# Optimization experiments

Measured on AMD Instinct MI355X. Metric: run time of the kernel, lower is better.

## Reference

```python
import jax, jax.numpy as jnp
import numpy as np
import math

B, LQ, S, D = 8, 4096, 77, 1024
H, HD = 16, 64
R, ALPHA = 192, 16.0
LORA_SCALE = ALPHA / R
N_SUBJ = 32


def setup_inputs() -> dict:
    key = jax.random.key(0)
    ks = jax.random.split(key, 16)
    w = 0.02
    return {
        "hidden_states": jax.random.normal(ks[0], (B, LQ, D), jnp.float32),
        "encoder_hidden_states": jax.random.normal(ks[1], (B, S, D), jnp.float32),
        "Wq": jax.random.normal(ks[2], (D, D), jnp.float32) * w,
        "Wk": jax.random.normal(ks[3], (D, D), jnp.float32) * w,
        "Wv": jax.random.normal(ks[4], (D, D), jnp.float32) * w,
        "Wo": jax.random.normal(ks[5], (D, D), jnp.float32) * w,
        "bo": jnp.zeros((D,), jnp.float32),
        "Ak": jax.random.normal(ks[6], (R, D), jnp.float32) * w,
        "Bk": jax.random.normal(ks[7], (D, R), jnp.float32) * w,
        "Av": jax.random.normal(ks[8], (R, D), jnp.float32) * w,
        "Bv": jax.random.normal(ks[9], (D, R), jnp.float32) * w,
        "Ao": jax.random.normal(ks[10], (R, D), jnp.float32) * w,
        "Bo": jax.random.normal(ks[11], (D, R), jnp.float32) * w,
        "cross_attn_scale_factor": jnp.ones((), jnp.float32),
        "subj_b": jax.random.randint(ks[12], (N_SUBJ,), 0, B, jnp.int32),
        "subj_n": jax.random.randint(ks[13], (N_SUBJ,), 0, S, jnp.int32),
    }


def _lora(x, A, Bm):
    # peft LoRA delta: scale * (x @ A^T) @ B^T
    return LORA_SCALE * ((x @ A.T) @ Bm.T)


def reference(hidden_states, encoder_hidden_states, Wq, Wk, Wv, Wo, bo,
              Ak, Bk, Av, Bv, Ao, Bo, cross_attn_scale_factor, subj_b, subj_n):
    hs, ehs = hidden_states, encoder_hidden_states
    # q_lora_updates_query=False -> query uses the base projection only
    q = hs @ Wq.T                                  # [B, LQ, D]
    k = ehs @ Wk.T + _lora(ehs, Ak, Bk)            # [B, S, D] (to_k_lora)
    v = ehs @ Wv.T + _lora(ehs, Av, Bv)            # [B, S, D] (to_v_lora)

    q = q.reshape(B, LQ, H, HD).transpose(0, 2, 1, 3)   # [B,H,LQ,HD]
    k = k.reshape(B, S, H, HD).transpose(0, 2, 1, 3)    # [B,H,S,HD]
    v = v.reshape(B, S, H, HD).transpose(0, 2, 1, 3)

    scale = 1.0 / math.sqrt(HD)
    attn_score = jnp.einsum('bhld,bhsd->bhls', q, k) * scale  # [B,H,LQ,S]

    # normalize_cross_attn: zero-center subject-token scores over query dim,
    # then rescale by the learned cross_attn_scale_factor.
    sub = attn_score[subj_b, :, :, subj_n]                    # [K,H,LQ]
    sub = (sub - sub.mean(axis=2, keepdims=True)) * cross_attn_scale_factor
    attn_score = attn_score.at[subj_b, :, :, subj_n].set(sub)

    attn_weight = jax.nn.softmax(attn_score, axis=-1)
    out = jnp.einsum('bhls,bhsd->bhld', attn_weight, v)       # [B,H,LQ,HD]
    out = out.transpose(0, 2, 1, 3).reshape(B, LQ, D)

    # to_out_lora: base out-proj (with bias) + LoRA delta; to_out[1] dropout = id
    out = out @ Wo.T + bo + _lora(out, Ao, Bo)
    return out
```

## Files before the change

kernel.cpp:

```cpp
#include <hip/hip_runtime.h>
#include <stdint.h>

#define B_     8
#define LQ_    4096
#define S_     77
#define SP_    80
#define D_     1024
#define H_     16
#define HD_    64
#define NC_    1280
#define NSUBJ_ 32

typedef __attribute__((ext_vector_type(4))) float  f4;
typedef __attribute__((ext_vector_type(8))) short  short8;
typedef __attribute__((ext_vector_type(8))) unsigned short us8;
typedef __attribute__((ext_vector_type(4))) unsigned short us4;

__device__ __forceinline__ unsigned short f2bf(float f) {
  union { float f; unsigned u; } x; x.f = f;
  unsigned r = x.u + 0x7FFFu + ((x.u >> 16) & 1u);
  return (unsigned short)(r >> 16);
}

__device__ __forceinline__ void gload16(const void* g, void* s) {
  __builtin_amdgcn_global_load_lds((const __attribute__((address_space(1))) void*)g,
                                   (__attribute__((address_space(3))) void*)s, 16, 0, 0);
}

__global__ __launch_bounds__(256) void k_hssum(const float* __restrict__ hs,
                                               float* __restrict__ part,
                                               unsigned short* __restrict__ hsb) {
  int b = blockIdx.y;
  size_t base = ((size_t)b * LQ_ + (size_t)blockIdx.x * 64) * D_ + threadIdx.x * 4;
  f4 acc = {0.f, 0.f, 0.f, 0.f};
  for (int l = 0; l < 64; ++l) {
    f4 v = *(const f4*)(hs + base + (size_t)l * D_);
    acc += v;
    if (hsb) {
      us4 o;
#pragma unroll
      for (int j = 0; j < 4; ++j) o[j] = f2bf(v[j]);
      *(us4*)(hsb + base + (size_t)l * D_) = o;
    }
  }
  *(f4*)(part + (size_t)blockIdx.x * (B_ * D_) + b * D_ + threadIdx.x * 4) = acc;
}

__global__ __launch_bounds__(256) void k_hsred(const float* __restrict__ part,
                                               float* __restrict__ hssum) {
  int i = blockIdx.x * 256 + threadIdx.x;
  float s = 0.f;
  for (int x = 0; x < 64; ++x) s += part[(size_t)x * (B_ * D_) + i];
  hssum[i] = s;
}

__global__ __launch_bounds__(256) void k_tr4(const float* __restrict__ Wq, const float* __restrict__ Ak,
                                             const float* __restrict__ Av, const float* __restrict__ Ao,
                                             float* __restrict__ wqT, float* __restrict__ akT,
                                             float* __restrict__ avT, float* __restrict__ aoT) {
  int z = blockIdx.z;
  const float* in = z == 0 ? Wq : (z == 1 ? Ak : (z == 2 ? Av : Ao));
  float* out = z == 0 ? wqT : (z == 1 ? akT : (z == 2 ? avT : aoT));
  int R = z == 0 ? 1024 : 192;
  const int C = 1024;
  int c0 = blockIdx.x * 32, r0 = blockIdx.y * 32;
  if (r0 >= R) return;
  __shared__ float tile[32][33];
  int tx = threadIdx.x & 31, ty = threadIdx.x >> 5;
#pragma unroll
  for (int k = 0; k < 4; ++k)
    tile[ty + 8 * k][tx] = in[(size_t)(r0 + ty + 8 * k) * C + c0 + tx];
  __syncthreads();
#pragma unroll
  for (int k = 0; k < 4; ++k)
    out[(size_t)(c0 + ty + 8 * k) * R + r0 + tx] = tile[tx][ty + 8 * k];
}

template <bool OBF>
__device__ __forceinline__ void gemm64_body(
    const float* __restrict__ A, int lda, const float* __restrict__ Bt, int ldb,
    void* __restrict__ Cv, int ldc, long cbase, const float* __restrict__ Dm, int ldd,
    int M, int Mv, int N, int K, float alpha, int m0, int n0,
    short* As, short* Bs) {
  int t = threadIdx.x, lane = t & 63, wid = t >> 6;
  int wm = wid >> 1, wn = wid & 1;
  f4 acc[2][2] = {};
  int srow = t >> 2, skc = (t & 3) * 8;
  for (int k0 = 0; k0 < K; k0 += 32) {
    __syncthreads();
    f4 a0 = {0,0,0,0}, a1 = {0,0,0,0}, b0 = {0,0,0,0}, b1 = {0,0,0,0};
    if (m0 + srow < Mv) {
      const float* p = A + (size_t)(m0 + srow) * lda + k0 + skc;
      a0 = *(const f4*)p; a1 = *(const f4*)(p + 4);
    }
    if (n0 + srow < N) {
      const float* p = Bt + (size_t)(n0 + srow) * ldb + k0 + skc;
      b0 = *(const f4*)p; b1 = *(const f4*)(p + 4);
    }
    us8 ua, ub;
#pragma unroll
    for (int j = 0; j < 4; ++j) {
      ua[j] = f2bf(a0[j]); ua[4 + j] = f2bf(a1[j]);
      ub[j] = f2bf(b0[j]); ub[4 + j] = f2bf(b1[j]);
    }
    *(us8*)(As + srow * 40 + skc) = ua;
    *(us8*)(Bs + srow * 40 + skc) = ub;
    __syncthreads();
    short8 fa[2], fb[2];
#pragma unroll
    for (int i = 0; i < 2; ++i) {
      fa[i] = *(const short8*)(As + (wm * 32 + i * 16 + (lane & 15)) * 40 + (lane >> 4) * 8);
      fb[i] = *(const short8*)(Bs + (wn * 32 + i * 16 + (lane & 15)) * 40 + (lane >> 4) * 8);
    }
#pragma unroll
    for (int mi = 0; mi < 2; ++mi)
#pragma unroll
      for (int ni = 0; ni < 2; ++ni)
        acc[mi][ni] = __builtin_amdgcn_mfma_f32_16x16x32_bf16(fa[mi], fb[ni], acc[mi][ni], 0, 0, 0);
  }
#pragma unroll
  for (int mi = 0; mi < 2; ++mi)
#pragma unroll
    for (int ni = 0; ni < 2; ++ni)
#pragma unroll
      for (int j = 0; j < 4; ++j) {
        int row = m0 + wm * 32 + mi * 16 + (lane >> 4) * 4 + j;
        int col = n0 + wn * 32 + ni * 16 + (lane & 15);
        if (row < M && col < N) {
          float val = acc[mi][ni][j] * alpha;
          if (Dm) val += Dm[(size_t)row * ldd + col];
          size_t idx = (size_t)cbase + (size_t)row * ldc + col;
          if (OBF) ((unsigned short*)Cv)[idx] = f2bf(val);
          else     ((float*)Cv)[idx] = val;
        }
      }
}

template <bool OBF>
__global__ __launch_bounds__(256) void k_gemm_small(
    const float* __restrict__ A, int lda, long sA1, long sA2,
    const float* __restrict__ Bt, int ldb, long sB1, long sB2,
    void* __restrict__ Cv, int ldc, long sC1, long sC2,
    const float* __restrict__ Dm, int ldd,
    int M, int Mv, int N, int K, float alpha, int Z2) {
  int z = blockIdx.z, z1 = z / Z2, z2 = z - z1 * Z2;
  __shared__ short As[64 * 40];
  __shared__ short Bs[64 * 40];
  gemm64_body<OBF>(A + z1 * sA1 + z2 * sA2, lda, Bt + z1 * sB1 + z2 * sB2, ldb,
                   Cv, ldc, z1 * sC1 + z2 * sC2, Dm, ldd, M, Mv, N, K, alpha,
                   blockIdx.x * 64, blockIdx.y * 64, As, Bs);
}

__global__ __launch_bounds__(256) void k_weff(
    const float* __restrict__ Bk, const float* __restrict__ Bv, const float* __restrict__ Bo,
    const float* __restrict__ akT, const float* __restrict__ avT, const float* __restrict__ aoT,
    const float* __restrict__ Wk, const float* __restrict__ Wv, const float* __restrict__ Wo,
    float* __restrict__ weff, float alpha) {
  int z = blockIdx.z;
  const float* A  = z == 0 ? Bk : (z == 1 ? Bv : Bo);
  const float* Bt = z == 0 ? akT : (z == 1 ? avT : aoT);
  const float* Dm = z == 0 ? Wk : (z == 1 ? Wv : Wo);
  __shared__ short As[64 * 40];
  __shared__ short Bs[64 * 40];
  gemm64_body<false>(A, 192, Bt, 192, weff + (size_t)z * 1048576, 1024, 0, Dm, 1024,
                     1024, 1024, 1024, 192, alpha, blockIdx.x * 64, blockIdx.y * 64, As, Bs);
}

__global__ void k_mubeta(const float* __restrict__ hssum, const float* __restrict__ Wq,
                         const float* __restrict__ kv,
                         const int* __restrict__ sb, const int* __restrict__ sn,
                         const float* __restrict__ csf_p,
                         float* __restrict__ alphav, float* __restrict__ betav) {
  int h = blockIdx.x, b = blockIdx.y;
  int t = threadIdx.x;
  __shared__ float qp[64];
  {
    int hd = t >> 1, half = t & 1;
    const float* wr = Wq + (size_t)(h * 64 + hd) * D_ + half * 512;
    const float* hp = hssum + b * D_ + half * 512;
    float s = 0.f;
    for (int d = 0; d < 512; d += 4) {
      f4 w = *(const f4*)(wr + d);
      f4 x = *(const f4*)(hp + d);
      s += w[0] * x[0] + w[1] * x[1] + w[2] * x[2] + w[3] * x[3];
    }
    s += __shfl_xor(s, 1, 64);
    if (half == 0) qp[hd] = s * (1.f / 4096.f);
  }
  __syncthreads();
  int s = t;
  if (s >= SP_) return;
  const float* kp = kv + ((size_t)(b * SP_ + s)) * 2048 + h * HD_;
  float mu = 0.f;
#pragma unroll 8
  for (int hd = 0; hd < HD_; ++hd) mu += qp[hd] * kp[hd];
  mu *= 0.125f;
  bool subj = false;
  for (int i = 0; i < NSUBJ_; ++i) subj = subj || (sb[i] == b && sn[i] == s);
  float csf = *csf_p;
  int c = b * NC_ + h * SP_ + s;
  alphav[c] = subj ? csf : 1.f;
  betav[c] = (s >= S_) ? -1e30f : (subj ? -mu * csf : 0.f);
}

__global__ __launch_bounds__(512, 2) void k_score_big(
    const unsigned short* __restrict__ hsb, const unsigned short* __restrict__ Mt,
    const float* __restrict__ alphav, const float* __restrict__ betav,
    unsigned short* __restrict__ P) {
  extern __shared__ short lds[];
  int id = blockIdx.x;
  int x = id & 7, idp = id >> 3;
  int nt = idp & 3;
  int pid = (idp >> 2) * 8 + x;
  int b = pid >> 4, mt = pid & 15;
  int m0 = mt * 256, n0 = nt * 320;

  const unsigned short* Ab = hsb + (size_t)b * LQ_ * D_;
  const unsigned short* Bb = Mt + (size_t)b * NC_ * D_;
  const float* alp = alphav + b * NC_;
  const float* bet = betav + b * NC_;
  unsigned short* Pb = P + (size_t)b * LQ_ * NC_;

  int t = threadIdx.x, lane = t & 63, wid = t >> 6;
  int wm = wid >> 2, wn = wid & 3;
  int r = lane & 15, q = lane >> 4;
  f4 acc[8][5] = {};

  auto SA = [&](int bf, int k0, int p) {
    int cb = p * 512 + wid * 64;
    int cc = cb + lane;
    int row = cc >> 2, gc = (cc & 3) ^ ((row >> 1) & 3);
    gload16(Ab + (size_t)(m0 + row) * D_ + k0 + gc * 8, (char*)(lds + bf * 8192) + cb * 16);
  };
  auto SB = [&](int bf, int k0, int p) {
    int cb = p * 512 + wid * 64;
    int cc = cb + lane;
    int row = cc >> 2, gc = (cc & 3) ^ ((row >> 1) & 3);
    gload16(Bb + (size_t)(n0 + row) * D_ + k0 + gc * 8, (char*)(lds + 32768 + bf * 10240) + cb * 16);
  };
  auto STAGE = [&](int bf, int k0) {
    SA(bf, k0, 0); SA(bf, k0, 1);
    SB(bf, k0, 0); SB(bf, k0, 1);
    if (wid < 4) { int cb = 1024 + wid * 64; int cc = cb + lane;
      int row = cc >> 2, gc = (cc & 3) ^ ((row >> 1) & 3);
      gload16(Bb + (size_t)(n0 + row) * D_ + k0 + gc * 8, (char*)(lds + 32768) + (size_t)bf * 20480 + cb * 16);
    }
  };

  const int T = 32;
  STAGE(0, 0); STAGE(1, 32); STAGE(2, 64);
  for (int kt = 0; kt < T; ++kt) {
    if (kt + 3 < T) {
      STAGE((kt + 3) & 3, (kt + 3) * 32);
      if (wid < 4) asm volatile("s_waitcnt vmcnt(15)" ::: "memory");
      else         asm volatile("s_waitcnt vmcnt(12)" ::: "memory");
    } else if (kt + 2 < T) {
      if (wid < 4) asm volatile("s_waitcnt vmcnt(10)" ::: "memory");
      else         asm volatile("s_waitcnt vmcnt(8)" ::: "memory");
    } else if (kt + 1 < T) {
      if (wid < 4) asm volatile("s_waitcnt vmcnt(5)" ::: "memory");
      else         asm volatile("s_waitcnt vmcnt(4)" ::: "memory");
    } else {
      asm volatile("s_waitcnt vmcnt(0)" ::: "memory");
    }
    __builtin_amdgcn_s_barrier();
    int cur = kt & 3;
    const short* Ar = lds + cur * 8192;
    const short* Br = lds + 32768 + cur * 10240;
    short8 fa[8], fb[5];
#pragma unroll
    for (int ni = 0; ni < 5; ++ni) {
      int row = wn * 80 + ni * 16 + r;
      fb[ni] = *(const short8*)(Br + row * 32 + ((q ^ ((row >> 1) & 3)) * 8));
    }
#pragma unroll
    for (int mi = 0; mi < 8; ++mi) {
      int row = wm * 128 + mi * 16 + r;
      fa[mi] = *(const short8*)(Ar + row * 32 + ((q ^ ((row >> 1) & 3)) * 8));
    }
    __builtin_amdgcn_s_setprio(1);
#pragma unroll
    for (int mi = 0; mi < 8; ++mi)
#pragma unroll
      for (int ni = 0; ni < 5; ++ni)
        acc[mi][ni] = __builtin_amdgcn_mfma_f32_16x16x32_bf16(fa[mi], fb[ni], acc[mi][ni], 0, 0, 0);
    __builtin_amdgcn_s_setprio(0);
    __builtin_amdgcn_s_barrier();
  }

  float al[5], be[5];
#pragma unroll
  for (int ni = 0; ni < 5; ++ni) {
    int cc = n0 + wn * 80 + ni * 16 + r;
    al[ni] = alp[cc]; be[ni] = bet[cc];
  }
#pragma unroll
  for (int mi = 0; mi < 8; ++mi) {
#pragma unroll
    for (int j = 0; j < 4; ++j) {
      float v[5];
      float m = -3.0e38f;
#pragma unroll
      for (int ni = 0; ni < 5; ++ni) { v[ni] = acc[mi][ni][j] * al[ni] + be[ni]; m = fmaxf(m, v[ni]); }
#pragma unroll
      for (int off = 1; off < 16; off <<= 1) m = fmaxf(m, __shfl_xor(m, off, 64));
      float ssum = 0.f;
#pragma unroll
      for (int ni = 0; ni < 5; ++ni) { v[ni] = __expf(v[ni] - m); ssum += v[ni]; }
#pragma unroll
      for (int off = 1; off < 16; off <<= 1) ssum += __shfl_xor(ssum, off, 64);
      float inv = 1.f / ssum;
      int row = m0 + wm * 128 + mi * 16 + q * 4 + j;
      size_t rb = (size_t)row * NC_ + n0 + wn * 80 + r;
#pragma unroll
      for (int ni = 0; ni < 5; ++ni)
        Pb[rb + ni * 16] = f2bf(v[ni] * inv);
    }
  }
}

__global__ __launch_bounds__(256) void k_score_f32(
    const float* __restrict__ hs, const unsigned short* __restrict__ Mt,
    const float* __restrict__ alphav, const float* __restrict__ betav,
    unsigned short* __restrict__ P) {
  int id = blockIdx.x;
  int x = id & 7, idp = id >> 3;
  int n_t = idp & 7;
  int pid = (idp >> 3) * 8 + x;
  int b = pid >> 5, m_t = pid & 31;
  int m0 = m_t * 128, n0 = n_t * 160;
  const float* Af = hs + (size_t)b * LQ_ * D_;
  const unsigned short* Bb = Mt + (size_t)b * NC_ * D_;
  const float* alp = alphav + b * NC_;
  const float* bet = betav + b * NC_;
  unsigned short* Pb = P + (size_t)b * LQ_ * NC_;
  __shared__ short As[128 * 64];
  __shared__ short Bs[160 * 64];
  int t = threadIdx.x, lane = t & 63, wid = t >> 6;
  int wm = wid >> 1, wn = wid & 1;
  int srow = lane >> 3;
  int schunk = (lane & 7) ^ srow;
  f4 acc[4][5] = {};
  for (int k0 = 0; k0 < D_; k0 += 64) {
    __syncthreads();
    for (int i = wid; i < 20; i += 4)
      gload16(Bb + (size_t)(n0 + i * 8 + srow) * D_ + k0 + schunk * 8, (char*)Bs + i * 1024);
    int arow = t >> 3, ac = t & 7;
    int awc = ac ^ (arow & 7);
#pragma unroll
    for (int p = 0; p < 4; ++p) {
      int row = p * 32 + arow;
      const float* src = Af + (size_t)(m0 + row) * D_ + k0 + ac * 8;
      f4 v0 = *(const f4*)src;
      f4 v1 = *(const f4*)(src + 4);
      us8 u;
#pragma unroll
      for (int j = 0; j < 4; ++j) { u[j] = f2bf(v0[j]); u[4 + j] = f2bf(v1[j]); }
      *(us8*)(As + row * 64 + awc * 8) = u;
    }
    __syncthreads();
#pragma unroll
    for (int kk = 0; kk < 2; ++kk) {
      int co = ((kk * 4 + (lane >> 4)) ^ (lane & 7)) * 8;
      short8 fa[4], fb[5];
#pragma unroll
      for (int mi = 0; mi < 4; ++mi)
        fa[mi] = *(const short8*)(As + (wm * 64 + mi * 16 + (lane & 15)) * 64 + co);
#pragma unroll
      for (int ni = 0; ni < 5; ++ni)
        fb[ni] = *(const short8*)(Bs + (wn * 80 + ni * 16 + (lane & 15)) * 64 + co);
#pragma unroll
      for (int mi = 0; mi < 4; ++mi)
#pragma unroll
        for (int ni = 0; ni < 5; ++ni)
          acc[mi][ni] = __builtin_amdgcn_mfma_f32_16x16x32_bf16(fa[mi], fb[ni], acc[mi][ni], 0, 0, 0);
    }
  }
  float al[5], be[5];
#pragma unroll
  for (int ni = 0; ni < 5; ++ni) {
    int cc = n0 + wn * 80 + ni * 16 + (lane & 15);
    al[ni] = alp[cc]; be[ni] = bet[cc];
  }
#pragma unroll
  for (int mi = 0; mi < 4; ++mi) {
#pragma unroll
    for (int j = 0; j < 4; ++j) {
      float v[5];
      float m = -3.0e38f;
#pragma unroll
      for (int ni = 0; ni < 5; ++ni) { v[ni] = acc[mi][ni][j] * al[ni] + be[ni]; m = fmaxf(m, v[ni]); }
#pragma unroll
      for (int off = 1; off < 16; off <<= 1) m = fmaxf(m, __shfl_xor(m, off, 64));
      float ssum = 0.f;
#pragma unroll
      for (int ni = 0; ni < 5; ++ni) { v[ni] = __expf(v[ni] - m); ssum += v[ni]; }
#pragma unroll
      for (int off = 1; off < 16; off <<= 1) ssum += __shfl_xor(ssum, off, 64);
      float inv = 1.f / ssum;
      int row = m0 + wm * 64 + mi * 16 + (lane >> 4) * 4 + j;
      size_t rb = (size_t)row * NC_ + n0 + wn * 80 + (lane & 15);
#pragma unroll
      for (int ni = 0; ni < 5; ++ni)
        Pb[rb + ni * 16] = f2bf(v[ni] * inv);
    }
  }
}

__global__ __launch_bounds__(512, 2) void k_out_big(
    const unsigned short* __restrict__ P, const unsigned short* __restrict__ Ut,
    const float* __restrict__ bo, float* __restrict__ out) {
  extern __shared__ short lds[];
  int id = blockIdx.x;
  int x = id & 7, idp = id >> 3;
  int nt = idp & 3;
  int pid = (idp >> 2) * 8 + x;
  int b = pid >> 4, mt = pid & 15;
  int m0 = mt * 256, n0 = nt * 256;

  const unsigned short* Ab = P + (size_t)b * LQ_ * NC_;
  const unsigned short* Bb = Ut + (size_t)b * D_ * NC_;
  float* ob = out + (size_t)b * LQ_ * D_;

  int t = threadIdx.x, lane = t & 63, wid = t >> 6;
  int wm = wid >> 2, wn = wid & 3;
  int r = lane & 15, q = lane >> 4;
  f4 acc[8][4] = {};
  const int T = NC_ / 32;

  auto SA = [&](int bf, int k0, int p) {
    int cb = p * 512 + wid * 64;
    int cc = cb + lane;
    int row = cc >> 2, gc = (cc & 3) ^ ((row >> 1) & 3);
    gload16(Ab + (size_t)(m0 + row) * NC_ + k0 + gc * 8, (char*)(lds + bf * 8192) + cb * 16);
  };
  auto SB = [&](int bf, int k0, int p) {
    int cb = p * 512 + wid * 64;
    int cc = cb + lane;
    int row = cc >> 2, gc = (cc & 3) ^ ((row >> 1) & 3);
    gload16(Bb + (size_t)(n0 + row) * NC_ + k0 + gc * 8, (char*)(lds + 32768 + bf * 8192) + cb * 16);
  };
  auto STAGE = [&](int bf, int k0) { SA(bf, k0, 0); SA(bf, k0, 1); SB(bf, k0, 0); SB(bf, k0, 1); };

  STAGE(0, 0); STAGE(1, 32); STAGE(2, 64);
  for (int kt = 0; kt < T; ++kt) {
    if (kt + 3 < T) {
      STAGE((kt + 3) & 3, (kt + 3) * 32);
      asm volatile("s_waitcnt vmcnt(12)" ::: "memory");
    } else if (kt + 2 < T) {
      asm volatile("s_waitcnt vmcnt(8)" ::: "memory");
    } else if (kt + 1 < T) {
      asm volatile("s_waitcnt vmcnt(4)" ::: "memory");
    } else {
      asm volatile("s_waitcnt vmcnt(0)" ::: "memory");
    }
    __builtin_amdgcn_s_barrier();
    int cur = kt & 3;
    const short* Ar = lds + cur * 8192;
    const short* Br = lds + 32768 + cur * 8192;
    short8 fa[8], fb[4];
#pragma unroll
    for (int ni = 0; ni < 4; ++ni) {
      int row = wn * 64 + ni * 16 + r;
      fb[ni] = *(const short8*)(Br + row * 32 + ((q ^ ((row >> 1) & 3)) * 8));
    }
#pragma unroll
    for (int mi = 0; mi < 8; ++mi) {
      int row = wm * 128 + mi * 16 + r;
      fa[mi] = *(const short8*)(Ar + row * 32 + ((q ^ ((row >> 1) & 3)) * 8));
    }
    __builtin_amdgcn_s_setprio(1);
#pragma unroll
    for (int mi = 0; mi < 8; ++mi)
#pragma unroll
      for (int ni = 0; ni < 4; ++ni)
        acc[mi][ni] = __builtin_amdgcn_mfma_f32_16x16x32_bf16(fa[mi], fb[ni], acc[mi][ni], 0, 0, 0);
    __builtin_amdgcn_s_setprio(0);
    __builtin_amdgcn_s_barrier();
  }

#pragma unroll
  for (int ni = 0; ni < 4; ++ni) {
    int col = n0 + wn * 64 + ni * 16 + r;
    float bov = bo[col];
#pragma unroll
    for (int mi = 0; mi < 8; ++mi)
#pragma unroll
      for (int j = 0; j < 4; ++j) {
        int row = m0 + wm * 128 + mi * 16 + q * 4 + j;
        ob[(size_t)row * D_ + col] = acc[mi][ni][j] + bov;
      }
  }
}

extern "C" void kernel_launch(void* const* d_in, const int* in_sizes, int n_in,
                              void* d_out, int out_size, void* d_ws, size_t ws_size,
                              hipStream_t stream) {
  const float* hs  = (const float*)d_in[0];
  const float* ehs = (const float*)d_in[1];
  const float* Wq  = (const float*)d_in[2];
  const float* Wk  = (const float*)d_in[3];
  const float* Wv  = (const float*)d_in[4];
  const float* Wo  = (const float*)d_in[5];
  const float* bo  = (const float*)d_in[6];
  const float* Ak  = (const float*)d_in[7];
  const float* Bk  = (const float*)d_in[8];
  const float* Av  = (const float*)d_in[9];
  const float* Bv  = (const float*)d_in[10];
  const float* Ao  = (const float*)d_in[11];
  const float* Bo  = (const float*)d_in[12];
  const float* csf = (const float*)d_in[13];
  const int*   sb  = (const int*)d_in[14];
  const int*   sn  = (const int*)d_in[15];
  float* out = (float*)d_out;

  hipFuncSetAttribute(reinterpret_cast<const void*>(k_score_big),
                      hipFuncAttributeMaxDynamicSharedMemorySize, 147456);
  hipFuncSetAttribute(reinterpret_cast<const void*>(k_out_big),
                      hipFuncAttributeMaxDynamicSharedMemorySize, 131072);

  char* ws = (char*)d_ws;
  unsigned short* P  = (unsigned short*)ws;
  unsigned short* Mt = (unsigned short*)(ws + 83886080);
  unsigned short* Ut = (unsigned short*)(ws + 104857600);
  const size_t NEED_HSB = 125829120ULL + 67108864ULL + 81920ULL;
  bool useHsb = ws_size >= NEED_HSB;
  unsigned short* hsb = useHsb ? (unsigned short*)(ws + 125829120) : nullptr;
  char* tail = useHsb ? (ws + 192937984) : (ws + 125829120);
  float* alphav = (float*)tail;
  float* betav  = (float*)(tail + 40960);
  float* kvbuf = (float*)(ws + 0);
  float* weff  = (float*)(ws + 5242880);
  float* wqT   = (float*)(ws + 17825792);
  float* aT    = (float*)(ws + 22020096);
  float* part  = (float*)(ws + 24379392);
  float* hssum = (float*)(ws + 26476544);

  float* woE = weff + 2097152;
  float* akT = aT;
  float* avT = aT + 196608;
  float* aoT = aT + 393216;

  const float LS = 16.0f / 192.0f;

  k_hssum<<<dim3(64, 8), 256, 0, stream>>>(hs, part, hsb);
  k_hsred<<<32, 256, 0, stream>>>(part, hssum);

  k_tr4<<<dim3(32, 32, 4), 256, 0, stream>>>(Wq, Ak, Av, Ao, wqT, akT, avT, aoT);

  k_weff<<<dim3(16, 16, 3), 256, 0, stream>>>(Bk, Bv, Bo, akT, avT, aoT, Wk, Wv, Wo, weff, LS);

  k_gemm_small<false><<<dim3(2, 32, 8), 256, 0, stream>>>(
      ehs, 1024, 77L * 1024, 0, weff, 1024, 0, 0, kvbuf, 2048, 80L * 2048, 0, nullptr, 0,
      80, 77, 2048, 1024, 1.f, 1);

  k_gemm_small<true><<<dim3(2, 16, 128), 256, 0, stream>>>(
      kvbuf, 2048, 80L * 2048, 64L, wqT, 1024, 0, 64L,
      Mt, 1024, (long)NC_ * 1024, 80L * 1024, nullptr, 0,
      80, 80, 1024, 64, 0.125f, 16);

  k_gemm_small<true><<<dim3(16, 2, 128), 256, 0, stream>>>(
      woE, 1024, 0, 64L, kvbuf + 1024, 2048, 80L * 2048, 64L,
      Ut, NC_, 1024L * NC_, 80L, nullptr, 0,
      1024, 1024, 80, 64, 1.f, 16);

  k_mubeta<<<dim3(16, 8), 128, 0, stream>>>(hssum, Wq, kvbuf, sb, sn, csf, alphav, betav);

  if (useHsb)
    k_score_big<<<512, 512, 147456, stream>>>(hsb, Mt, alphav, betav, P);
  else
    k_score_f32<<<2048, 256, 0, stream>>>(hs, Mt, alphav, betav, P);
  k_out_big<<<512, 512, 131072, stream>>>(P, Ut, bo, out);

  (void)in_sizes; (void)n_in; (void)out_size; (void)ws_size;
}
```

Measured before the change: 377.5 us.

## Split GEMM main loops into two interleaved phases with staged global prefetch

Both bf16 MFMA GEMM main loops now run each K-step as two half-phases. Each phase loads half of the A fragments from LDS, issues part of the next global-to-LDS prefetch, and runs the MFMAs for that half, with barriers between phases. The aim is to overlap LDS reads, global loads and MFMA work better and to lower register pressure by holding 4 A fragments instead of 8. The cost is extra barriers per iteration and hand-tuned vmcnt counts that must match exactly to stay correct.

```diff
diff --git a/kernel.cpp b/kernel.cpp
--- a/kernel.cpp
+++ b/kernel.cpp
@@ -238,54 +238,82 @@
     int row = cc >> 2, gc = (cc & 3) ^ ((row >> 1) & 3);
     gload16(Bb + (size_t)(n0 + row) * D_ + k0 + gc * 8, (char*)(lds + 32768 + bf * 10240) + cb * 16);
   };
-  auto STAGE = [&](int bf, int k0) {
-    SA(bf, k0, 0); SA(bf, k0, 1);
-    SB(bf, k0, 0); SB(bf, k0, 1);
-    if (wid < 4) { int cb = 1024 + wid * 64; int cc = cb + lane;
+  auto SBx = [&](int bf, int k0) {
+    if (wid < 4) {
+      int cb = 1024 + wid * 64;
+      int cc = cb + lane;
       int row = cc >> 2, gc = (cc & 3) ^ ((row >> 1) & 3);
-      gload16(Bb + (size_t)(n0 + row) * D_ + k0 + gc * 8, (char*)(lds + 32768) + (size_t)bf * 20480 + cb * 16);
+      gload16(Bb + (size_t)(n0 + row) * D_ + k0 + gc * 8, (char*)(lds + 32768 + bf * 10240) + cb * 16);
     }
   };
-
-  const int T = 32;
-  STAGE(0, 0); STAGE(1, 32); STAGE(2, 64);
-  for (int kt = 0; kt < T; ++kt) {
-    if (kt + 3 < T) {
-      STAGE((kt + 3) & 3, (kt + 3) * 32);
-      if (wid < 4) asm volatile("s_waitcnt vmcnt(15)" ::: "memory");
-      else         asm volatile("s_waitcnt vmcnt(12)" ::: "memory");
-    } else if (kt + 2 < T) {
-      if (wid < 4) asm volatile("s_waitcnt vmcnt(10)" ::: "memory");
-      else         asm volatile("s_waitcnt vmcnt(8)" ::: "memory");
-    } else if (kt + 1 < T) {
-      if (wid < 4) asm volatile("s_waitcnt vmcnt(5)" ::: "memory");
-      else         asm volatile("s_waitcnt vmcnt(4)" ::: "memory");
-    } else {
-      asm volatile("s_waitcnt vmcnt(0)" ::: "memory");
-    }
-    __builtin_amdgcn_s_barrier();
-    int cur = kt & 3;
-    const short* Ar = lds + cur * 8192;
-    const short* Br = lds + 32768 + cur * 10240;
-    short8 fa[8], fb[5];
+  auto STAGE_P1 = [&](int h) { if (h < 32) { int bf = h & 3, k0 = h * 32; SA(bf, k0, 0); SA(bf, k0, 1); SB(bf, k0, 0); } };
+  auto STAGE_P2 = [&](int h) { if (h < 32) { int bf = h & 3, k0 = h * 32; SB(bf, k0, 1); SBx(bf, k0); } };
+
+  STAGE_P1(0); STAGE_P2(0);
+  STAGE_P1(1); STAGE_P2(1);
+  STAGE_P1(2); STAGE_P2(2);
+  if (wid < 4) asm volatile("s_waitcnt vmcnt(10)" ::: "memory");
+  else         asm volatile("s_waitcnt vmcnt(8)" ::: "memory");
+  __builtin_amdgcn_s_barrier();
+
+#pragma unroll 1
+  for (int h = 0; h < 32; ++h) {
+    int bf = h & 3;
+    const short* Ar = lds + bf * 8192;
+    const short* Br = lds + 32768 + bf * 10240;
+    short8 fa[4], fb[5];
+
 #pragma unroll
     for (int ni = 0; ni < 5; ++ni) {
       int row = wn * 80 + ni * 16 + r;
       fb[ni] = *(const short8*)(Br + row * 32 + ((q ^ ((row >> 1) & 3)) * 8));
     }
 #pragma unroll
-    for (int mi = 0; mi < 8; ++mi) {
+    for (int mi = 0; mi < 4; ++mi) {
       int row = wm * 128 + mi * 16 + r;
       fa[mi] = *(const short8*)(Ar + row * 32 + ((q ^ ((row >> 1) & 3)) * 8));
     }
+    __builtin_amdgcn_sched_barrier(0);
+    STAGE_P1(h + 3);
+    __builtin_amdgcn_sched_barrier(0);
+    __builtin_amdgcn_s_barrier();
+    asm volatile("s_waitcnt lgkmcnt(0)");
     __builtin_amdgcn_s_setprio(1);
 #pragma unroll
-    for (int mi = 0; mi < 8; ++mi)
+    for (int mi = 0; mi < 4; ++mi)
 #pragma unroll
       for (int ni = 0; ni < 5; ++ni)
         acc[mi][ni] = __builtin_amdgcn_mfma_f32_16x16x32_bf16(fa[mi], fb[ni], acc[mi][ni], 0, 0, 0);
     __builtin_amdgcn_s_setprio(0);
+
+#pragma unroll
+    for (int mi = 0; mi < 4; ++mi) {
+      int row = wm * 128 + (4 + mi) * 16 + r;
+      fa[mi] = *(const short8*)(Ar + row * 32 + ((q ^ ((row >> 1) & 3)) * 8));
+    }
+    __builtin_amdgcn_sched_barrier(0);
+    STAGE_P2(h + 3);
+    __builtin_amdgcn_sched_barrier(0);
     __builtin_amdgcn_s_barrier();
+    asm volatile("s_waitcnt lgkmcnt(0)");
+    __builtin_amdgcn_s_setprio(1);
+#pragma unroll
+    for (int mi = 0; mi < 4; ++mi)
+#pragma unroll
+      for (int ni = 0; ni < 5; ++ni)
+        acc[4 + mi][ni] = __builtin_amdgcn_mfma_f32_16x16x32_bf16(fa[mi], fb[ni], acc[4 + mi][ni], 0, 0, 0);
+    __builtin_amdgcn_s_setprio(0);
+
+    if (h <= 28) {
+      if (wid < 4) asm volatile("s_waitcnt vmcnt(10)" ::: "memory");
+      else         asm volatile("s_waitcnt vmcnt(8)" ::: "memory");
+    } else if (h == 29) {
+      if (wid < 4) asm volatile("s_waitcnt vmcnt(5)" ::: "memory");
+      else         asm volatile("s_waitcnt vmcnt(4)" ::: "memory");
+    } else if (h == 30) {
+      asm volatile("s_waitcnt vmcnt(0)" ::: "memory");
+    }
+    if (h < 31) __builtin_amdgcn_s_barrier();
   }
 
   float al[5], be[5];
@@ -440,43 +468,71 @@
     int row = cc >> 2, gc = (cc & 3) ^ ((row >> 1) & 3);
     gload16(Bb + (size_t)(n0 + row) * NC_ + k0 + gc * 8, (char*)(lds + 32768 + bf * 8192) + cb * 16);
   };
-  auto STAGE = [&](int bf, int k0) { SA(bf, k0, 0); SA(bf, k0, 1); SB(bf, k0, 0); SB(bf, k0, 1); };
-
-  STAGE(0, 0); STAGE(1, 32); STAGE(2, 64);
-  for (int kt = 0; kt < T; ++kt) {
-    if (kt + 3 < T) {
-      STAGE((kt + 3) & 3, (kt + 3) * 32);
-      asm volatile("s_waitcnt vmcnt(12)" ::: "memory");
-    } else if (kt + 2 < T) {
-      asm volatile("s_waitcnt vmcnt(8)" ::: "memory");
-    } else if (kt + 1 < T) {
-      asm volatile("s_waitcnt vmcnt(4)" ::: "memory");
-    } else {
-      asm volatile("s_waitcnt vmcnt(0)" ::: "memory");
-    }
-    __builtin_amdgcn_s_barrier();
-    int cur = kt & 3;
-    const short* Ar = lds + cur * 8192;
-    const short* Br = lds + 32768 + cur * 8192;
-    short8 fa[8], fb[4];
+  auto STAGE_P1 = [&](int h) { if (h < T) { int bf = h & 3, k0 = h * 32; SA(bf, k0, 0); SA(bf, k0, 1); } };
+  auto STAGE_P2 = [&](int h) { if (h < T) { int bf = h & 3, k0 = h * 32; SB(bf, k0, 0); SB(bf, k0, 1); } };
+
+  STAGE_P1(0); STAGE_P2(0);
+  STAGE_P1(1); STAGE_P2(1);
+  STAGE_P1(2); STAGE_P2(2);
+  asm volatile("s_waitcnt vmcnt(8)" ::: "memory");
+  __builtin_amdgcn_s_barrier();
+
+#pragma unroll 1
+  for (int h = 0; h < T; ++h) {
+    int bf = h & 3;
+    const short* Ar = lds + bf * 8192;
+    const short* Br = lds + 32768 + bf * 8192;
+    short8 fa[4], fb[4];
+
 #pragma unroll
     for (int ni = 0; ni < 4; ++ni) {
       int row = wn * 64 + ni * 16 + r;
       fb[ni] = *(const short8*)(Br + row * 32 + ((q ^ ((row >> 1) & 3)) * 8));
     }
 #pragma unroll
-    for (int mi = 0; mi < 8; ++mi) {
+    for (int mi = 0; mi < 4; ++mi) {
       int row = wm * 128 + mi * 16 + r;
       fa[mi] = *(const short8*)(Ar + row * 32 + ((q ^ ((row >> 1) & 3)) * 8));
     }
+    __builtin_amdgcn_sched_barrier(0);
+    STAGE_P1(h + 3);
+    __builtin_amdgcn_sched_barrier(0);
+    __builtin_amdgcn_s_barrier();
+    asm volatile("s_waitcnt lgkmcnt(0)");
     __builtin_amdgcn_s_setprio(1);
 #pragma unroll
-    for (int mi = 0; mi < 8; ++mi)
+    for (int mi = 0; mi < 4; ++mi)
 #pragma unroll
       for (int ni = 0; ni < 4; ++ni)
         acc[mi][ni] = __builtin_amdgcn_mfma_f32_16x16x32_bf16(fa[mi], fb[ni], acc[mi][ni], 0, 0, 0);
     __builtin_amdgcn_s_setprio(0);
+
+#pragma unroll
+    for (int mi = 0; mi < 4; ++mi) {
+      int row = wm * 128 + (4 + mi) * 16 + r;
+      fa[mi] = *(const short8*)(Ar + row * 32 + ((q ^ ((row >> 1) & 3)) * 8));
+    }
+    __builtin_amdgcn_sched_barrier(0);
+    STAGE_P2(h + 3);
+    __builtin_amdgcn_sched_barrier(0);
     __builtin_amdgcn_s_barrier();
+    asm volatile("s_waitcnt lgkmcnt(0)");
+    __builtin_amdgcn_s_setprio(1);
+#pragma unroll
+    for (int mi = 0; mi < 4; ++mi)
+#pragma unroll
+      for (int ni = 0; ni < 4; ++ni)
+        acc[4 + mi][ni] = __builtin_amdgcn_mfma_f32_16x16x32_bf16(fa[mi], fb[ni], acc[4 + mi][ni], 0, 0, 0);
+    __builtin_amdgcn_s_setprio(0);
+
+    if (h <= T - 4) {
+      asm volatile("s_waitcnt vmcnt(8)" ::: "memory");
+    } else if (h == T - 3) {
+      asm volatile("s_waitcnt vmcnt(4)" ::: "memory");
+    } else if (h == T - 2) {
+      asm volatile("s_waitcnt vmcnt(0)" ::: "memory");
+    }
+    if (h < T - 1) __builtin_amdgcn_s_barrier();
   }
 
 #pragma unroll
```

New measurement: 373.4 us. About the same (-1.1%).
